# Kernel optimization log

Hardware: AMD Instinct MI355X
Metric: run time of the kernel (lower is better)

The kernel has to match this reference:

```python
import jax, jax.numpy as jnp
import numpy as np

D_MODEL = 1024
STATE_DIM = 256


def setup_inputs() -> dict:
    key = jax.random.key(0)
    k_u, k_lam, k_B, k_C = jax.random.split(key, 4)
    u = jax.random.normal(k_u, (4, 4096, D_MODEL), dtype=jnp.float32)
    # log_lambda ~ N(3.0, 0.5^2), matching torch.randn(state_dim)*0.5 + 3.0
    log_lambda = jax.random.normal(k_lam, (STATE_DIM,), dtype=jnp.float32) * 0.5 + 3.0
    # torch Linear weights: B.weight [state_dim, d_model], C.weight [d_model, state_dim]
    B_w = jax.random.normal(k_B, (STATE_DIM, D_MODEL), dtype=jnp.float32) / np.sqrt(D_MODEL)
    C_w = jax.random.normal(k_C, (D_MODEL, STATE_DIM), dtype=jnp.float32) / np.sqrt(STATE_DIM)
    D = jnp.zeros((D_MODEL,), dtype=jnp.float32)
    return {"u": u, "log_lambda": log_lambda, "B_w": B_w, "C_w": C_w, "D": D}


def reference(u, log_lambda, B_w, C_w, D):
    # u: [batch, seq, d_model]
    lam = jax.nn.sigmoid(log_lambda)                      # [state_dim]
    Bu = jnp.einsum('bsd,nd->bsn', u, B_w)                # [batch, seq, state_dim]

    def step(h, bu_t):
        h = lam * h + bu_t                                # [batch, state_dim]
        return h, h

    h0 = jnp.zeros((u.shape[0], lam.shape[0]), dtype=u.dtype)
    # scan over time axis; Bu transposed to [seq, batch, state_dim]
    _, hs = jax.lax.scan(step, h0, jnp.swapaxes(Bu, 0, 1))
    hs = jnp.swapaxes(hs, 0, 1)                           # [batch, seq, state_dim]
    y = jnp.einsum('bsn,dn->bsd', hs, C_w) + D * u        # [batch, seq, d_model]
    return y
```

## Files before the change

### kernel.cpp

```cpp
#include <hip/hip_runtime.h>
#include <math.h>

typedef unsigned short ushort_t;
typedef __bf16 v8bf __attribute__((ext_vector_type(8)));
typedef __bf16 v4bf __attribute__((ext_vector_type(4)));
typedef float  v4f  __attribute__((ext_vector_type(4)));
typedef float  f32x4 __attribute__((ext_vector_type(4)));

#define BATCH 4
#define SEQ 4096
#define DM 1024
#define NS 256
#define MROWS (BATCH*SEQ)

#define NCH 128
#define CL (SEQ/NCH)

#define BK1 64
#define BM2 32
#define BK2 64

typedef __attribute__((address_space(1))) void as1_void;
typedef __attribute__((address_space(3))) void as3_void;

__device__ __forceinline__ void gl_lds16(const void* g, void* l) {
    __builtin_amdgcn_global_load_lds((as1_void*)g, (as3_void*)l, 16, 0, 0);
}

__device__ __forceinline__ ushort_t f2bf(float f) {
    unsigned u = __builtin_bit_cast(unsigned, f);
    u += 0x7fff + ((u >> 16) & 1);
    return (ushort_t)(u >> 16);
}

__device__ __forceinline__ float sigm(float x) { return 1.0f / (1.0f + expf(-x)); }

__device__ __forceinline__ float powk(int e, float l1, float l2, float l4,
                                      float l8, float l16) {
    float w = 1.0f;
    if (e & 1)  w *= l1;
    if (e & 2)  w *= l2;
    if (e & 4)  w *= l4;
    if (e & 8)  w *= l8;
    if (e & 16) w *= l16;
    return w;
}

__global__ __launch_bounds__(256)
void gemm1_fused(const float* __restrict__ A,
                 const ushort_t* __restrict__ B,
                 float* __restrict__ Bu,
                 const float* __restrict__ ll,
                 float* __restrict__ cf)
{
    const int K = DM;
    __shared__ __align__(16) ushort_t As[2][32*BK1];
    __shared__ __align__(16) ushort_t Bs[2][NS*BK1];

    const int tid  = threadIdx.x;
    const int lane = tid & 63;
    const int wave = tid >> 6;
    const int m0   = blockIdx.x * 32;

    const int fr = lane & 15;
    const int fq = lane >> 4;

    int arow[2], ac4[2], aoff[2];
    #pragma unroll
    for (int j = 0; j < 2; ++j) {
        int cid = j*256 + tid;
        arow[j] = cid >> 4;
        ac4[j]  = (cid & 15) * 4;
        aoff[j] = arow[j]*BK1 + (((ac4[j] >> 3) ^ (arow[j] & 7)) * 8) + (ac4[j] & 4);
    }
    int brow[8], bcs[8];
    #pragma unroll
    for (int j = 0; j < 8; ++j) {
        int cid = j*256 + tid;
        brow[j] = cid >> 3;
        bcs[j]  = ((cid & 7) ^ (brow[j] & 7)) * 8;
    }

    f32x4 acc[2][4] = {};
    v4f areg0[2], areg1[2];

    const int NIT = K / BK1;

    #pragma unroll
    for (int j = 0; j < 2; ++j)
        areg0[j] = *(const v4f*)&A[(size_t)(m0 + arow[j])*K + ac4[j]];
    #pragma unroll
    for (int j = 0; j < 8; ++j)
        gl_lds16(&B[(size_t)brow[j]*K + bcs[j]], &Bs[0][(j*256 + tid)*8]);
    #pragma unroll
    for (int j = 0; j < 2; ++j)
        areg1[j] = *(const v4f*)&A[(size_t)(m0 + arow[j])*K + BK1 + ac4[j]];

    #define G1_STEP(IT, P, AREG)                                               \
    {                                                                          \
        _Pragma("unroll")                                                      \
        for (int j = 0; j < 2; ++j)                                            \
            *(v4bf*)&As[P][aoff[j]] = __builtin_convertvector(AREG[j], v4bf);  \
        __syncthreads();                                                       \
        if ((IT) + 2 < NIT) {                                                  \
            const int k2 = ((IT) + 2) * BK1;                                   \
            _Pragma("unroll")                                                  \
            for (int j = 0; j < 2; ++j)                                        \
                AREG[j] = *(const v4f*)&A[(size_t)(m0 + arow[j])*K + k2 + ac4[j]]; \
        }                                                                      \
        if ((IT) + 1 < NIT) {                                                  \
            const int k1 = ((IT) + 1) * BK1;                                   \
            _Pragma("unroll")                                                  \
            for (int j = 0; j < 8; ++j)                                        \
                gl_lds16(&B[(size_t)brow[j]*K + k1 + bcs[j]],                  \
                         &Bs[(P)^1][(j*256 + tid)*8]);                         \
        }                                                                      \
        _Pragma("unroll")                                                      \
        for (int kk = 0; kk < 2; ++kk) {                                       \
            v8bf af[2], bf[4];                                                 \
            _Pragma("unroll")                                                  \
            for (int mi = 0; mi < 2; ++mi) {                                   \
                const int r  = mi*16 + fr;                                     \
                const int ch = (kk*4 + fq) ^ (r & 7);                          \
                af[mi] = *reinterpret_cast<const v8bf*>(&As[P][r*BK1 + ch*8]); \
            }                                                                  \
            _Pragma("unroll")                                                  \
            for (int ni = 0; ni < 4; ++ni) {                                   \
                const int r  = wave*64 + ni*16 + fr;                           \
                const int ch = (kk*4 + fq) ^ (r & 7);                          \
                bf[ni] = *reinterpret_cast<const v8bf*>(&Bs[P][r*BK1 + ch*8]); \
            }                                                                  \
            _Pragma("unroll")                                                  \
            for (int mi = 0; mi < 2; ++mi)                                     \
                _Pragma("unroll")                                              \
                for (int ni = 0; ni < 4; ++ni)                                 \
                    acc[mi][ni] = __builtin_amdgcn_mfma_f32_16x16x32_bf16(     \
                                      af[mi], bf[ni], acc[mi][ni], 0, 0, 0);   \
        }                                                                      \
    }

    for (int it = 0; it < NIT; it += 2) {
        G1_STEP(it,     0, areg0);
        G1_STEP(it + 1, 1, areg1);
    }
    #undef G1_STEP

    #pragma unroll
    for (int mi = 0; mi < 2; ++mi) {
        #pragma unroll
        for (int ni = 0; ni < 4; ++ni) {
            const int col = wave*64 + ni*16 + fr;
            #pragma unroll
            for (int r = 0; r < 4; ++r)
                Bu[(size_t)(m0 + mi*16 + fq*4 + r)*NS + col] = acc[mi][ni][r];
        }
    }

    const int b_idx = m0 >> 12;
    const int c_idx = (m0 & 4095) >> 5;

    #pragma unroll
    for (int ni = 0; ni < 4; ++ni) {
        const int col = wave*64 + ni*16 + fr;
        const float l1  = sigm(ll[col]);
        const float l2  = l1*l1;
        const float l4  = l2*l2;
        const float l8  = l4*l4;
        const float l16 = l8*l8;
        float f = 0.0f;
        #pragma unroll
        for (int mi = 0; mi < 2; ++mi) {
            float w = powk(28 - mi*16 - fq*4, l1, l2, l4, l8, l16);
            f = fmaf(w, acc[mi][ni][3], f);
            w *= l1; f = fmaf(w, acc[mi][ni][2], f);
            w *= l1; f = fmaf(w, acc[mi][ni][1], f);
            w *= l1; f = fmaf(w, acc[mi][ni][0], f);
        }
        f += __shfl_xor(f, 16, 64);
        f += __shfl_xor(f, 32, 64);
        if (fq == 0)
            cf[((size_t)b_idx*NCH + c_idx)*NS + col] = f;
    }
}

__global__ __launch_bounds__(256)
void gemm2_scan(const float* __restrict__ Bu,
                const ushort_t* __restrict__ Cw,
                const float* __restrict__ ll,
                const float* __restrict__ cf,
                float* __restrict__ Y,
                const float* __restrict__ Dvec,
                const float* __restrict__ U)
{
    __shared__ __align__(16) ushort_t hsS[BM2*NS];
    __shared__ __align__(16) ushort_t Bsw[2][128*BK2];

    const int tid  = threadIdx.x;
    const int lane = tid & 63;
    const int wave = tid >> 6;
    const int fr = lane & 15;
    const int fq = lane >> 4;
    const int m0 = blockIdx.x * BM2;
    const int n  = tid;

    const float* bp = Bu + (size_t)m0*NS + n;
    float v[CL];
    #pragma unroll
    for (int t = 0; t < CL; ++t)
        v[t] = bp[(size_t)t*NS];

    #define STAGE_B(g, buf)                                                    \
        {                                                                      \
            const int p_ = (g) >> 2, ks_ = (g) & 3;                            \
            _Pragma("unroll")                                                  \
            for (int jj = 0; jj < 4; ++jj) {                                   \
                const int cid = jj*256 + tid;                                  \
                const int row_ = cid >> 3, kch_ = cid & 7;                     \
                const int koff_ = ks_*BK2 + ((kch_ ^ (row_ & 7)) * 8);         \
                gl_lds16(&Cw[(size_t)(p_*128 + row_)*NS + koff_],              \
                         &Bsw[buf][cid*8]);                                    \
            }                                                                  \
        }
    STAGE_B(0, 0);

    const int b_idx = m0 >> 12;
    const int cG    = (m0 & 4095) >> 5;
    const float lam = sigm(ll[n]);
    float lamL = lam;
    #pragma unroll
    for (int i = 0; i < 5; ++i) lamL *= lamL;

    const float* cfb = cf + (size_t)b_idx*NCH*NS + n;
    float x = 0.0f;
    int cc = 0;
    for (; cc + 16 <= cG; cc += 16) {
        float vv[16];
        #pragma unroll
        for (int j = 0; j < 16; ++j) vv[j] = cfb[(size_t)(cc + j)*NS];
        #pragma unroll
        for (int j = 0; j < 16; ++j) x = fmaf(lamL, x, vv[j]);
    }
    for (; cc < cG; ++cc) x = fmaf(lamL, x, cfb[(size_t)cc*NS]);

    float h = x;
    #pragma unroll
    for (int t = 0; t < CL; ++t) {
        h = fmaf(lam, h, v[t]);
        hsS[t*NS + (((n >> 3) ^ (t & 7)) << 3) + (n & 7)] = f2bf(h);
    }
    __syncthreads();

    int g = 0;
    for (int p = 0; p < 8; ++p) {
        f32x4 acc[2][2] = {};
        for (int ks = 0; ks < 4; ++ks, ++g) {
            const int cur = g & 1;
            if (g) __syncthreads();
            if (g + 1 < 32) STAGE_B(g + 1, cur ^ 1);

            #pragma unroll
            for (int kk = 0; kk < 2; ++kk) {
                v8bf af[2], bf[2];
                #pragma unroll
                for (int mi = 0; mi < 2; ++mi) {
                    const int r  = mi*16 + fr;
                    const int ch = (ks*8 + kk*4 + fq) ^ (r & 7);
                    af[mi] = *reinterpret_cast<const v8bf*>(&hsS[r*NS + ch*8]);
                }
                #pragma unroll
                for (int ni = 0; ni < 2; ++ni) {
                    const int rn = wave*32 + ni*16 + fr;
                    const int ch = (kk*4 + fq) ^ (rn & 7);
                    bf[ni] = *reinterpret_cast<const v8bf*>(&Bsw[cur][rn*BK2 + ch*8]);
                }
                #pragma unroll
                for (int mi = 0; mi < 2; ++mi)
                    #pragma unroll
                    for (int ni = 0; ni < 2; ++ni)
                        acc[mi][ni] = __builtin_amdgcn_mfma_f32_16x16x32_bf16(
                                          af[mi], bf[ni], acc[mi][ni], 0, 0, 0);
            }
        }
        #pragma unroll
        for (int ni = 0; ni < 2; ++ni) {
            const int gcol = p*128 + wave*32 + ni*16 + fr;
            const float d = Dvec[gcol];
            #pragma unroll
            for (int mi = 0; mi < 2; ++mi) {
                #pragma unroll
                for (int r = 0; r < 4; ++r) {
                    const int grow = m0 + mi*16 + fq*4 + r;
                    const size_t idx = (size_t)grow*DM + gcol;
                    float vo = acc[mi][ni][r];
                    if (d != 0.0f) vo = fmaf(d, U[idx], vo);
                    Y[idx] = vo;
                }
            }
        }
    }
    #undef STAGE_B
}

__global__ __launch_bounds__(256)
void cvt_w(const float4* __restrict__ Bw, const float4* __restrict__ Cw,
           ushort_t* __restrict__ Bo, ushort_t* __restrict__ Co)
{
    const int i = blockIdx.x * 256 + threadIdx.x;
    const float4* src = blockIdx.y ? Cw : Bw;
    ushort_t*     dst = blockIdx.y ? Co : Bo;
    float4 v = src[i];
    ushort4 o;
    o.x = f2bf(v.x); o.y = f2bf(v.y); o.z = f2bf(v.z); o.w = f2bf(v.w);
    *(ushort4*)&dst[4*(size_t)i] = o;
}

extern "C" void kernel_launch(void* const* d_in, const int* in_sizes, int n_in,
                              void* d_out, int out_size, void* d_ws, size_t ws_size,
                              hipStream_t stream) {
    const float* u          = (const float*)d_in[0];
    const float* log_lambda = (const float*)d_in[1];
    const float* B_w        = (const float*)d_in[2];
    const float* C_w        = (const float*)d_in[3];
    const float* Dv         = (const float*)d_in[4];
    float* y  = (float*)d_out;

    char* w = (char*)d_ws;
    float*    Bu   = (float*)w;
    ushort_t* Bw16 = (ushort_t*)(w + 16777216);
    ushort_t* Cw16 = (ushort_t*)(w + 17301504);
    float*    cf   = (float*)(w + 17825792);

    dim3 blk(256);

    cvt_w<<<dim3(256, 2), blk, 0, stream>>>((const float4*)B_w, (const float4*)C_w,
                                            Bw16, Cw16);

    gemm1_fused<<<dim3(MROWS/32), blk, 0, stream>>>(u, Bw16, Bu, log_lambda, cf);

    gemm2_scan<<<dim3(MROWS/BM2), blk, 0, stream>>>(
        Bu, Cw16, log_lambda, cf, y, Dv, u);
}
```

Before: 163.1 us.

## Load weight fragments directly from global memory instead of LDS staging in both GEMMs

Both GEMM kernels stop staging the bf16 weight matrices (B_w in gemm1, C_w in gemm2) through double-buffered shared memory. Each wave now reads its MFMA B-fragments straight from global memory, relying on L2/L1 since the weights are small and shared by all blocks. This removes the LDS copies and the per-stage barriers in gemm2, cuts LDS use so more blocks can fit per CU, and lets each gemm2 wave own a contiguous 256-column slice with larger 2x4 tiles. The cost is global-load latency sitting directly in the MFMA loop with no prefetch, plus uncoalesced 16-byte row-strided reads.

```diff
diff --git a/kernel.cpp b/kernel.cpp
--- a/kernel.cpp
+++ b/kernel.cpp
@@ -18,7 +18,6 @@
 
 #define BK1 64
 #define BM2 32
-#define BK2 64
 
 typedef __attribute__((address_space(1))) void as1_void;
 typedef __attribute__((address_space(3))) void as3_void;
@@ -55,7 +54,6 @@
 {
     const int K = DM;
     __shared__ __align__(16) ushort_t As[2][32*BK1];
-    __shared__ __align__(16) ushort_t Bs[2][NS*BK1];
 
     const int tid  = threadIdx.x;
     const int lane = tid & 63;
@@ -73,25 +71,17 @@
         ac4[j]  = (cid & 15) * 4;
         aoff[j] = arow[j]*BK1 + (((ac4[j] >> 3) ^ (arow[j] & 7)) * 8) + (ac4[j] & 4);
     }
-    int brow[8], bcs[8];
-    #pragma unroll
-    for (int j = 0; j < 8; ++j) {
-        int cid = j*256 + tid;
-        brow[j] = cid >> 3;
-        bcs[j]  = ((cid & 7) ^ (brow[j] & 7)) * 8;
-    }
 
     f32x4 acc[2][4] = {};
     v4f areg0[2], areg1[2];
 
     const int NIT = K / BK1;
 
+    const ushort_t* Bq = B + (size_t)(wave*64 + fr)*K + fq*8;
+
     #pragma unroll
     for (int j = 0; j < 2; ++j)
         areg0[j] = *(const v4f*)&A[(size_t)(m0 + arow[j])*K + ac4[j]];
-    #pragma unroll
-    for (int j = 0; j < 8; ++j)
-        gl_lds16(&B[(size_t)brow[j]*K + bcs[j]], &Bs[0][(j*256 + tid)*8]);
     #pragma unroll
     for (int j = 0; j < 2; ++j)
         areg1[j] = *(const v4f*)&A[(size_t)(m0 + arow[j])*K + BK1 + ac4[j]];
@@ -108,13 +98,6 @@
             for (int j = 0; j < 2; ++j)                                        \
                 AREG[j] = *(const v4f*)&A[(size_t)(m0 + arow[j])*K + k2 + ac4[j]]; \
         }                                                                      \
-        if ((IT) + 1 < NIT) {                                                  \
-            const int k1 = ((IT) + 1) * BK1;                                   \
-            _Pragma("unroll")                                                  \
-            for (int j = 0; j < 8; ++j)                                        \
-                gl_lds16(&B[(size_t)brow[j]*K + k1 + bcs[j]],                  \
-                         &Bs[(P)^1][(j*256 + tid)*8]);                         \
-        }                                                                      \
         _Pragma("unroll")                                                      \
         for (int kk = 0; kk < 2; ++kk) {                                       \
             v8bf af[2], bf[4];                                                 \
@@ -125,11 +108,9 @@
                 af[mi] = *reinterpret_cast<const v8bf*>(&As[P][r*BK1 + ch*8]); \
             }                                                                  \
             _Pragma("unroll")                                                  \
-            for (int ni = 0; ni < 4; ++ni) {                                   \
-                const int r  = wave*64 + ni*16 + fr;                           \
-                const int ch = (kk*4 + fq) ^ (r & 7);                          \
-                bf[ni] = *reinterpret_cast<const v8bf*>(&Bs[P][r*BK1 + ch*8]); \
-            }                                                                  \
+            for (int ni = 0; ni < 4; ++ni)                                     \
+                bf[ni] = *reinterpret_cast<const v8bf*>(                       \
+                    &Bq[(size_t)ni*16*K + (IT)*BK1 + kk*32]);                  \
             _Pragma("unroll")                                                  \
             for (int mi = 0; mi < 2; ++mi)                                     \
                 _Pragma("unroll")                                              \
@@ -193,7 +174,6 @@
                 const float* __restrict__ U)
 {
     __shared__ __align__(16) ushort_t hsS[BM2*NS];
-    __shared__ __align__(16) ushort_t Bsw[2][128*BK2];
 
     const int tid  = threadIdx.x;
     const int lane = tid & 63;
@@ -209,20 +189,6 @@
     for (int t = 0; t < CL; ++t)
         v[t] = bp[(size_t)t*NS];
 
-    #define STAGE_B(g, buf)                                                    \
-        {                                                                      \
-            const int p_ = (g) >> 2, ks_ = (g) & 3;                            \
-            _Pragma("unroll")                                                  \
-            for (int jj = 0; jj < 4; ++jj) {                                   \
-                const int cid = jj*256 + tid;                                  \
-                const int row_ = cid >> 3, kch_ = cid & 7;                     \
-                const int koff_ = ks_*BK2 + ((kch_ ^ (row_ & 7)) * 8);         \
-                gl_lds16(&Cw[(size_t)(p_*128 + row_)*NS + koff_],              \
-                         &Bsw[buf][cid*8]);                                    \
-            }                                                                  \
-        }
-    STAGE_B(0, 0);
-
     const int b_idx = m0 >> 12;
     const int cG    = (m0 & 4095) >> 5;
     const float lam = sigm(ll[n]);
@@ -250,40 +216,33 @@
     }
     __syncthreads();
 
-    int g = 0;
-    for (int p = 0; p < 8; ++p) {
-        f32x4 acc[2][2] = {};
-        for (int ks = 0; ks < 4; ++ks, ++g) {
-            const int cur = g & 1;
-            if (g) __syncthreads();
-            if (g + 1 < 32) STAGE_B(g + 1, cur ^ 1);
-
-            #pragma unroll
-            for (int kk = 0; kk < 2; ++kk) {
-                v8bf af[2], bf[2];
+    const ushort_t* Cq = Cw + (size_t)(wave*256 + fr)*NS + fq*8;
+
+    for (int sl = 0; sl < 4; ++sl) {
+        f32x4 acc[2][4] = {};
+        #pragma unroll
+        for (int kk = 0; kk < 8; ++kk) {
+            v8bf af[2], bf[4];
+            #pragma unroll
+            for (int mi = 0; mi < 2; ++mi) {
+                const int r  = mi*16 + fr;
+                const int ch = (kk*4 + fq) ^ (r & 7);
+                af[mi] = *reinterpret_cast<const v8bf*>(&hsS[r*NS + ch*8]);
+            }
+            #pragma unroll
+            for (int ni = 0; ni < 4; ++ni)
+                bf[ni] = *reinterpret_cast<const v8bf*>(
+                    &Cq[(size_t)(sl*64 + ni*16)*NS + kk*32]);
+            #pragma unroll
+            for (int mi = 0; mi < 2; ++mi)
                 #pragma unroll
-                for (int mi = 0; mi < 2; ++mi) {
-                    const int r  = mi*16 + fr;
-                    const int ch = (ks*8 + kk*4 + fq) ^ (r & 7);
-                    af[mi] = *reinterpret_cast<const v8bf*>(&hsS[r*NS + ch*8]);
-                }
-                #pragma unroll
-                for (int ni = 0; ni < 2; ++ni) {
-                    const int rn = wave*32 + ni*16 + fr;
-                    const int ch = (kk*4 + fq) ^ (rn & 7);
-                    bf[ni] = *reinterpret_cast<const v8bf*>(&Bsw[cur][rn*BK2 + ch*8]);
-                }
-                #pragma unroll
-                for (int mi = 0; mi < 2; ++mi)
-                    #pragma unroll
-                    for (int ni = 0; ni < 2; ++ni)
-                        acc[mi][ni] = __builtin_amdgcn_mfma_f32_16x16x32_bf16(
-                                          af[mi], bf[ni], acc[mi][ni], 0, 0, 0);
-            }
+                for (int ni = 0; ni < 4; ++ni)
+                    acc[mi][ni] = __builtin_amdgcn_mfma_f32_16x16x32_bf16(
+                                      af[mi], bf[ni], acc[mi][ni], 0, 0, 0);
         }
         #pragma unroll
-        for (int ni = 0; ni < 2; ++ni) {
-            const int gcol = p*128 + wave*32 + ni*16 + fr;
+        for (int ni = 0; ni < 4; ++ni) {
+            const int gcol = wave*256 + sl*64 + ni*16 + fr;
             const float d = Dvec[gcol];
             #pragma unroll
             for (int mi = 0; mi < 2; ++mi) {
@@ -298,7 +257,6 @@
             }
         }
     }
-    #undef STAGE_B
 }
 
 __global__ __launch_bounds__(256)
```

Result: slower. 187.4 us (+14.9%).
